# Performance work log

Measured on AMD Instinct MI355X. Metric: run time of the kernel, lower is better.

Reference implementation:

```python
import jax, jax.numpy as jnp
import numpy as np

N = 50000      # num nodes
E = 600000     # num edges (avg degree 12)
IN = 256       # in_feats
H = 128        # h_feats
P = 2          # prop_step
LN_EPS = 1e-5


def setup_inputs() -> dict:
    key = jax.random.key(0)
    ks = jax.random.split(key, 8)
    return {
        "in_feat": jax.random.normal(ks[0], (N, IN), jnp.float32),
        "row": jax.random.randint(ks[1], (E,), 0, N),  # target node of each edge
        "col": jax.random.randint(ks[2], (E,), 0, N),  # source node of each edge
        "lin_w": jax.random.normal(ks[3], (H, IN), jnp.float32) / np.sqrt(IN).astype(np.float32),
        "lin_b": jnp.zeros((H,), jnp.float32),
        "conv_w": jax.random.normal(ks[4], (H, H), jnp.float32) / np.sqrt(H).astype(np.float32),
        "conv_b": jnp.zeros((H,), jnp.float32),
        "root_emb": jax.random.normal(ks[5], (1, H), jnp.float32) * 0.02,
        "ln_gamma": jnp.ones((P, H), jnp.float32),
        "ln_beta": jnp.zeros((P, H), jnp.float32),
    }


def _layernorm(x, g, b):
    mu = jnp.mean(x, axis=-1, keepdims=True)
    var = jnp.mean(jnp.square(x - mu), axis=-1, keepdims=True)
    return (x - mu) * jax.lax.rsqrt(var + LN_EPS) * g + b


def reference(in_feat, row, col, lin_w, lin_b, conv_w, conv_b, root_emb, ln_gamma, ln_beta):
    n = in_feat.shape[0]
    h = in_feat @ lin_w.T + lin_b                      # [N, H]

    # OGB-style degree norm with +1 trick (original edges, row = target)
    deg = jax.ops.segment_sum(jnp.ones_like(row, dtype=h.dtype), row, num_segments=n) + 1.0
    deg_inv = 1.0 / deg                                # deg >= 1, never inf

    # GCNConv symmetric norm with self loops: D^-1/2 (A+I) D^-1/2
    loop = jnp.arange(n)
    r2 = jnp.concatenate([row, loop])                  # [E+N] targets
    c2 = jnp.concatenate([col, loop])                  # [E+N] sources
    d2 = jax.ops.segment_sum(jnp.ones_like(r2, dtype=h.dtype), r2, num_segments=n)
    dis = jnp.where(d2 > 0, jax.lax.rsqrt(jnp.maximum(d2, 1.0)), 0.0)
    ew = dis[r2] * dis[c2]                             # [E+N] edge weights

    root = root_emb[0]                                 # [H]
    ori = h
    for i in range(P):
        if i != 0:
            h = h + ori                                # residual
            h = _layernorm(h, ln_gamma[i], ln_beta[i])
            h = jax.nn.relu(h)
            # dropout=0.0 -> identity
        xw = h @ conv_w.T                              # [N, H]
        h_msg = jax.ops.segment_sum(ew[:, None] * xw[c2], r2, num_segments=n) + conv_b
        root_contrib = jax.nn.relu(h + root) * deg_inv[:, None]
        h = h_msg + root_contrib
    return h
```

## Files before the change

kernel.cpp:

```cpp
#include <hip/hip_runtime.h>

#define NN 50000
#define EE 600000
#define INF 256
#define HF 128

typedef __attribute__((ext_vector_type(8))) short short8;
typedef __attribute__((ext_vector_type(4))) float floatx4;

__device__ __forceinline__ unsigned short f32_to_bf16_rne(float x) {
    unsigned int u = __float_as_uint(x);
    unsigned int r = (u + 0x7FFFu + ((u >> 16) & 1u)) >> 16;
    return (unsigned short)r;
}
__device__ __forceinline__ float bf16_to_f32(unsigned short h) {
    return __uint_as_float(((unsigned int)h) << 16);
}
__device__ __forceinline__ float bf16lo_u32(unsigned int u) {
    return __uint_as_float(u << 16);
}
__device__ __forceinline__ float bf16hi_u32(unsigned int u) {
    return __uint_as_float(u & 0xFFFF0000u);
}

__global__ void count_deg(const int* __restrict__ row, int* __restrict__ cnt, int E) {
    int e = blockIdx.x * blockDim.x + threadIdx.x;
    if (e < E) atomicAdd(&cnt[row[e]], 1);
}

__global__ void scan_phase1(const int* __restrict__ cnt, int* __restrict__ bsum, int n) {
    __shared__ int sdata[256];
    int t = threadIdx.x;
    int i = blockIdx.x * 256 + t;
    sdata[t] = (i < n) ? cnt[i] : 0;
    __syncthreads();
    for (int s = 128; s > 0; s >>= 1) {
        if (t < s) sdata[t] += sdata[t + s];
        __syncthreads();
    }
    if (t == 0) bsum[blockIdx.x] = sdata[0];
}

__global__ void scan_phase2(int* __restrict__ bsum, int nb) {
    __shared__ int sdata[256];
    int t = threadIdx.x;
    int v = (t < nb) ? bsum[t] : 0;
    sdata[t] = v;
    __syncthreads();
    for (int s = 1; s < 256; s <<= 1) {
        int add = (t >= s) ? sdata[t - s] : 0;
        __syncthreads();
        sdata[t] += add;
        __syncthreads();
    }
    if (t < nb) bsum[t] = sdata[t] - v;
}

__global__ void scan_phase3(const int* __restrict__ cnt, const int* __restrict__ bsum,
                            int* __restrict__ row_start, int* __restrict__ fill_pos,
                            float* __restrict__ deg_inv, float* __restrict__ dis,
                            int n, int E) {
    __shared__ int sdata[256];
    int t = threadIdx.x;
    int i = blockIdx.x * 256 + t;
    int v = (i < n) ? cnt[i] : 0;
    sdata[t] = v;
    __syncthreads();
    for (int s = 1; s < 256; s <<= 1) {
        int add = (t >= s) ? sdata[t - s] : 0;
        __syncthreads();
        sdata[t] += add;
        __syncthreads();
    }
    if (i < n) {
        int ex = bsum[blockIdx.x] + sdata[t] - v;
        row_start[i] = ex;
        fill_pos[i] = ex;
        float d = (float)(v + 1);
        deg_inv[i] = 1.0f / d;
        dis[i] = rsqrtf(d);
    }
    if (blockIdx.x == 0 && t == 0) row_start[n] = E;
}

__global__ void fill_csr(const int* __restrict__ row, const int* __restrict__ col,
                         const float* __restrict__ dis, int* __restrict__ fill_pos,
                         int* __restrict__ csr_col, float* __restrict__ csr_wc, int E) {
    int e = blockIdx.x * blockDim.x + threadIdx.x;
    if (e < E) {
        int r = row[e];
        int c = col[e];
        int p = atomicAdd(&fill_pos[r], 1);
        csr_col[p] = c;
        csr_wc[p] = dis[c];
    }
}

__global__ void prepack_w(const float* __restrict__ lw, const float* __restrict__ cw,
                          unsigned short* __restrict__ wlh, unsigned short* __restrict__ wll,
                          unsigned short* __restrict__ wch, unsigned short* __restrict__ wcl) {
    int idx = blockIdx.x * blockDim.x + threadIdx.x;
    const float* src;
    unsigned short *dh, *dl;
    int i;
    if (idx < 8192) {
        src = lw; dh = wlh; dl = wll; i = idx;
    } else if (idx < 12288) {
        src = cw; dh = wch; dl = wcl; i = idx - 8192;
    } else return;
    float4 v = *reinterpret_cast<const float4*>(&src[i * 4]);
    unsigned short hx = f32_to_bf16_rne(v.x), hy = f32_to_bf16_rne(v.y),
                   hz = f32_to_bf16_rne(v.z), hw = f32_to_bf16_rne(v.w);
    ushort4 hp = {hx, hy, hz, hw};
    ushort4 lp = {f32_to_bf16_rne(v.x - bf16_to_f32(hx)), f32_to_bf16_rne(v.y - bf16_to_f32(hy)),
                  f32_to_bf16_rne(v.z - bf16_to_f32(hz)), f32_to_bf16_rne(v.w - bf16_to_f32(hw))};
    *reinterpret_cast<ushort4*>(&dh[i * 4]) = hp;
    *reinterpret_cast<ushort4*>(&dl[i * 4]) = lp;
}

template <int K, int MODE>
__global__ __launch_bounds__(256) void gemm_mfma(
    const float* __restrict__ Af,
    const unsigned short* __restrict__ Ahg, const unsigned short* __restrict__ Alg,
    const unsigned short* __restrict__ Whg, const unsigned short* __restrict__ Wlg,
    const float* __restrict__ bias,
    float* __restrict__ C, unsigned short* __restrict__ Cbf,
    const float* __restrict__ h, const float* __restrict__ deg_inv,
    const float* __restrict__ root,
    const float* __restrict__ gamma, const float* __restrict__ beta,
    int M) {
    constexpr int LDA = 40;
    __shared__ unsigned short Ah[64 * LDA];
    __shared__ unsigned short Al[64 * LDA];
    __shared__ unsigned short Wh[128 * LDA];
    __shared__ unsigned short Wl[128 * LDA];

    const int t = threadIdx.x;
    const int bm = blockIdx.x * 64;
    const int wave = t >> 6;
    const int lane = t & 63;
    const int lrow = lane & 15;
    const int quad = lane >> 4;
    const int kbase = quad * 8;

    floatx4 acc[8];
#pragma unroll
    for (int nt = 0; nt < 8; ++nt) acc[nt] = (floatx4){0.f, 0.f, 0.f, 0.f};

    for (int k0 = 0; k0 < K; k0 += 32) {
        if (MODE == 0) {
#pragma unroll
            for (int r = 0; r < 2; ++r) {
                int f = t + 256 * r;
                int rw = f >> 3;
                int cq = f & 7;
                float4 v = make_float4(0.f, 0.f, 0.f, 0.f);
                int gr = bm + rw;
                if (gr < M) v = *reinterpret_cast<const float4*>(&Af[(size_t)gr * K + k0 + cq * 4]);
                unsigned short hx = f32_to_bf16_rne(v.x), hy = f32_to_bf16_rne(v.y),
                               hz = f32_to_bf16_rne(v.z), hw = f32_to_bf16_rne(v.w);
                unsigned short lx = f32_to_bf16_rne(v.x - bf16_to_f32(hx)),
                               ly = f32_to_bf16_rne(v.y - bf16_to_f32(hy)),
                               lz = f32_to_bf16_rne(v.z - bf16_to_f32(hz)),
                               lw = f32_to_bf16_rne(v.w - bf16_to_f32(hw));
                uint2 hp, lp;
                hp.x = (unsigned)hx | ((unsigned)hy << 16);
                hp.y = (unsigned)hz | ((unsigned)hw << 16);
                lp.x = (unsigned)lx | ((unsigned)ly << 16);
                lp.y = (unsigned)lz | ((unsigned)lw << 16);
                *reinterpret_cast<uint2*>(&Ah[rw * LDA + cq * 4]) = hp;
                *reinterpret_cast<uint2*>(&Al[rw * LDA + cq * 4]) = lp;
            }
        } else {
            int rw = t >> 2;
            int cq = t & 3;
            int gr = bm + rw;
            uint4 hv = make_uint4(0, 0, 0, 0), lv = make_uint4(0, 0, 0, 0);
            if (gr < M) {
                hv = *reinterpret_cast<const uint4*>(&Ahg[(size_t)gr * K + k0 + cq * 8]);
                lv = *reinterpret_cast<const uint4*>(&Alg[(size_t)gr * K + k0 + cq * 8]);
            }
            *reinterpret_cast<uint2*>(&Ah[rw * LDA + cq * 8]) = make_uint2(hv.x, hv.y);
            *reinterpret_cast<uint2*>(&Ah[rw * LDA + cq * 8 + 4]) = make_uint2(hv.z, hv.w);
            *reinterpret_cast<uint2*>(&Al[rw * LDA + cq * 8]) = make_uint2(lv.x, lv.y);
            *reinterpret_cast<uint2*>(&Al[rw * LDA + cq * 8 + 4]) = make_uint2(lv.z, lv.w);
        }
#pragma unroll
        for (int r = 0; r < 2; ++r) {
            int f = t + 256 * r;
            int rw = f >> 2;
            int cq = f & 3;
            uint4 hv = *reinterpret_cast<const uint4*>(&Whg[(size_t)rw * K + k0 + cq * 8]);
            uint4 lv = *reinterpret_cast<const uint4*>(&Wlg[(size_t)rw * K + k0 + cq * 8]);
            *reinterpret_cast<uint2*>(&Wh[rw * LDA + cq * 8]) = make_uint2(hv.x, hv.y);
            *reinterpret_cast<uint2*>(&Wh[rw * LDA + cq * 8 + 4]) = make_uint2(hv.z, hv.w);
            *reinterpret_cast<uint2*>(&Wl[rw * LDA + cq * 8]) = make_uint2(lv.x, lv.y);
            *reinterpret_cast<uint2*>(&Wl[rw * LDA + cq * 8 + 4]) = make_uint2(lv.z, lv.w);
        }
        __syncthreads();

        short8 afh = *reinterpret_cast<const short8*>(&Ah[(wave * 16 + lrow) * LDA + kbase]);
        short8 afl = *reinterpret_cast<const short8*>(&Al[(wave * 16 + lrow) * LDA + kbase]);
        short8 bfh[8], bfl[8];
#pragma unroll
        for (int nt = 0; nt < 8; ++nt) {
            int rw = nt * 16 + lrow;
            bfh[nt] = *reinterpret_cast<const short8*>(&Wh[rw * LDA + kbase]);
            bfl[nt] = *reinterpret_cast<const short8*>(&Wl[rw * LDA + kbase]);
        }
#pragma unroll
        for (int nt = 0; nt < 8; ++nt) {
            acc[nt] = __builtin_amdgcn_mfma_f32_16x16x32_bf16(afh, bfh[nt], acc[nt], 0, 0, 0);
            acc[nt] = __builtin_amdgcn_mfma_f32_16x16x32_bf16(afl, bfh[nt], acc[nt], 0, 0, 0);
            acc[nt] = __builtin_amdgcn_mfma_f32_16x16x32_bf16(afh, bfl[nt], acc[nt], 0, 0, 0);
        }
        __syncthreads();
    }

    float cb[8], rt[8], gm[8], bt[8];
#pragma unroll
    for (int nt = 0; nt < 8; ++nt) {
        int colh = nt * 16 + lrow;
        cb[nt] = bias[colh];
        if (MODE >= 1) rt[nt] = root[colh];
        if (MODE == 1) { gm[nt] = gamma[colh]; bt[nt] = beta[colh]; }
    }

#pragma unroll
    for (int r = 0; r < 4; ++r) {
        int grow = bm + wave * 16 + quad * 4 + r;
        if (grow >= M) continue;
        float x[8];
        if (MODE == 0) {
#pragma unroll
            for (int nt = 0; nt < 8; ++nt) x[nt] = acc[nt][r] + cb[nt];
        } else {
            float di = deg_inv[grow];
            float hv[8];
#pragma unroll
            for (int nt = 0; nt < 8; ++nt) hv[nt] = h[(size_t)grow * HF + nt * 16 + lrow];
#pragma unroll
            for (int nt = 0; nt < 8; ++nt) {
                float v = acc[nt][r] + cb[nt] + fmaxf(hv[nt] + rt[nt], 0.f) * di;
                x[nt] = (MODE == 1) ? v + hv[nt] : v;
            }
        }
        if (MODE == 1) {
            float s = 0.f;
#pragma unroll
            for (int nt = 0; nt < 8; ++nt) s += x[nt];
#pragma unroll
            for (int m = 1; m < 16; m <<= 1) s += __shfl_xor(s, m, 64);
            float mu = s * (1.0f / HF);
            float var = 0.f;
#pragma unroll
            for (int nt = 0; nt < 8; ++nt) { float d = x[nt] - mu; var += d * d; }
#pragma unroll
            for (int m = 1; m < 16; m <<= 1) var += __shfl_xor(var, m, 64);
            float rs = rsqrtf(var * (1.0f / HF) + 1e-5f);
#pragma unroll
            for (int nt = 0; nt < 8; ++nt) {
                int colh = nt * 16 + lrow;
                float y = fmaxf((x[nt] - mu) * rs * gm[nt] + bt[nt], 0.f);
                C[(size_t)grow * HF + colh] = y;
                Cbf[(size_t)grow * HF + colh] = f32_to_bf16_rne(y);
            }
        } else if (MODE == 0) {
#pragma unroll
            for (int nt = 0; nt < 8; ++nt) {
                int colh = nt * 16 + lrow;
                C[(size_t)grow * HF + colh] = x[nt];
                Cbf[(size_t)grow * HF + colh] = f32_to_bf16_rne(x[nt]);
            }
        } else {
#pragma unroll
            for (int nt = 0; nt < 8; ++nt)
                C[(size_t)grow * HF + nt * 16 + lrow] = x[nt];
        }
    }
}

__global__ void aggregate(const int* __restrict__ row_start, const int* __restrict__ csr_col,
                          const float* __restrict__ csr_wc, const float* __restrict__ dis,
                          const float* __restrict__ deg_inv, const float* __restrict__ h,
                          const unsigned short* __restrict__ hbf,
                          unsigned short* __restrict__ agg_hi, unsigned short* __restrict__ agg_lo,
                          int n) {
    int wid = (blockIdx.x * blockDim.x + threadIdx.x) >> 6;
    int lane = threadIdx.x & 63;
    if (wid >= n) return;
    int q = lane >> 4;
    int l16 = lane & 15;
    int s = row_start[wid];
    int e = row_start[wid + 1];
    float a0 = 0.f, a1 = 0.f, a2 = 0.f, a3 = 0.f, a4 = 0.f, a5 = 0.f, a6 = 0.f, a7 = 0.f;
    for (int j = s + q; j < e; j += 4) {
        int c = csr_col[j];
        float wc = csr_wc[j];
        uint4 hv = *reinterpret_cast<const uint4*>(&hbf[(size_t)c * HF + l16 * 8]);
        a0 = fmaf(wc, bf16lo_u32(hv.x), a0);
        a1 = fmaf(wc, bf16hi_u32(hv.x), a1);
        a2 = fmaf(wc, bf16lo_u32(hv.y), a2);
        a3 = fmaf(wc, bf16hi_u32(hv.y), a3);
        a4 = fmaf(wc, bf16lo_u32(hv.z), a4);
        a5 = fmaf(wc, bf16hi_u32(hv.z), a5);
        a6 = fmaf(wc, bf16lo_u32(hv.w), a6);
        a7 = fmaf(wc, bf16hi_u32(hv.w), a7);
    }
#pragma unroll
    for (int m = 16; m < 64; m <<= 1) {
        a0 += __shfl_xor(a0, m, 64);
        a1 += __shfl_xor(a1, m, 64);
        a2 += __shfl_xor(a2, m, 64);
        a3 += __shfl_xor(a3, m, 64);
        a4 += __shfl_xor(a4, m, 64);
        a5 += __shfl_xor(a5, m, 64);
        a6 += __shfl_xor(a6, m, 64);
        a7 += __shfl_xor(a7, m, 64);
    }
    if (q == 0) {
        float dn = dis[wid];
        float di = deg_inv[wid];
        float4 hA = *reinterpret_cast<const float4*>(&h[(size_t)wid * HF + l16 * 8]);
        float4 hB = *reinterpret_cast<const float4*>(&h[(size_t)wid * HF + l16 * 8 + 4]);
        float o[8];
        o[0] = fmaf(dn, a0, di * hA.x);
        o[1] = fmaf(dn, a1, di * hA.y);
        o[2] = fmaf(dn, a2, di * hA.z);
        o[3] = fmaf(dn, a3, di * hA.w);
        o[4] = fmaf(dn, a4, di * hB.x);
        o[5] = fmaf(dn, a5, di * hB.y);
        o[6] = fmaf(dn, a6, di * hB.z);
        o[7] = fmaf(dn, a7, di * hB.w);
        unsigned short hi[8], lo[8];
#pragma unroll
        for (int k = 0; k < 8; ++k) {
            hi[k] = f32_to_bf16_rne(o[k]);
            lo[k] = f32_to_bf16_rne(o[k] - bf16_to_f32(hi[k]));
        }
        uint4 hp, lp;
        hp.x = (unsigned)hi[0] | ((unsigned)hi[1] << 16);
        hp.y = (unsigned)hi[2] | ((unsigned)hi[3] << 16);
        hp.z = (unsigned)hi[4] | ((unsigned)hi[5] << 16);
        hp.w = (unsigned)hi[6] | ((unsigned)hi[7] << 16);
        lp.x = (unsigned)lo[0] | ((unsigned)lo[1] << 16);
        lp.y = (unsigned)lo[2] | ((unsigned)lo[3] << 16);
        lp.z = (unsigned)lo[4] | ((unsigned)lo[5] << 16);
        lp.w = (unsigned)lo[6] | ((unsigned)lo[7] << 16);
        *reinterpret_cast<uint4*>(&agg_hi[(size_t)wid * HF + l16 * 8]) = hp;
        *reinterpret_cast<uint4*>(&agg_lo[(size_t)wid * HF + l16 * 8]) = lp;
    }
}

extern "C" void kernel_launch(void* const* d_in, const int* in_sizes, int n_in,
                              void* d_out, int out_size, void* d_ws, size_t ws_size,
                              hipStream_t stream) {
    const int N = NN, E = EE;
    const float* in_feat = (const float*)d_in[0];
    const int* row = (const int*)d_in[1];
    const int* col = (const int*)d_in[2];
    const float* lin_w = (const float*)d_in[3];
    const float* lin_b = (const float*)d_in[4];
    const float* conv_w = (const float*)d_in[5];
    const float* conv_b = (const float*)d_in[6];
    const float* root_emb = (const float*)d_in[7];
    const float* ln_gamma = (const float*)d_in[8];
    const float* ln_beta = (const float*)d_in[9];
    float* out = (float*)d_out;

    float* ws = (float*)d_ws;
    float* deg_inv = ws;
    float* dis = deg_inv + N;
    int* cnt = (int*)(dis + N);
    int* row_start = cnt + N;
    int* fill_pos = row_start + N + 4;
    int* bsum = fill_pos + N;
    int* csr_col = bsum + 256;
    float* csr_wc = (float*)(csr_col + E);
    unsigned short* wlh = (unsigned short*)(csr_wc + E);
    unsigned short* wll = wlh + 32768;
    unsigned short* wch = wll + 32768;
    unsigned short* wcl = wch + 16384;
    float* h0 = (float*)(wcl + 16384);
    unsigned short* hbf = (unsigned short*)(h0 + (size_t)N * HF);
    unsigned short* agg_hi = hbf + (size_t)N * HF;
    unsigned short* agg_lo = agg_hi + (size_t)N * HF;

    const int NB = (N + 255) / 256;

    hipMemsetAsync(cnt, 0, N * sizeof(int), stream);
    count_deg<<<(E + 255) / 256, 256, 0, stream>>>(row, cnt, E);
    scan_phase1<<<NB, 256, 0, stream>>>(cnt, bsum, N);
    scan_phase2<<<1, 256, 0, stream>>>(bsum, NB);
    scan_phase3<<<NB, 256, 0, stream>>>(cnt, bsum, row_start, fill_pos, deg_inv, dis, N, E);
    fill_csr<<<(E + 255) / 256, 256, 0, stream>>>(row, col, dis, fill_pos, csr_col, csr_wc, E);
    prepack_w<<<48, 256, 0, stream>>>(lin_w, conv_w, wlh, wll, wch, wcl);

    const int GB = (N + 63) / 64;
    const int WB = (N + 3) / 4;

    gemm_mfma<INF, 0><<<GB, 256, 0, stream>>>(in_feat, nullptr, nullptr, wlh, wll, lin_b,
                                              h0, hbf, nullptr, nullptr, nullptr,
                                              nullptr, nullptr, N);

    aggregate<<<WB, 256, 0, stream>>>(row_start, csr_col, csr_wc, dis, deg_inv, h0, hbf,
                                      agg_hi, agg_lo, N);
    gemm_mfma<HF, 1><<<GB, 256, 0, stream>>>(nullptr, agg_hi, agg_lo, wch, wcl, conv_b,
                                             h0, hbf, h0, deg_inv, root_emb,
                                             ln_gamma + HF, ln_beta + HF, N);

    aggregate<<<WB, 256, 0, stream>>>(row_start, csr_col, csr_wc, dis, deg_inv, h0, hbf,
                                      agg_hi, agg_lo, N);
    gemm_mfma<HF, 2><<<GB, 256, 0, stream>>>(nullptr, agg_hi, agg_lo, wch, wcl, conv_b,
                                             out, nullptr, h0, deg_inv, root_emb,
                                             nullptr, nullptr, N);
}
```

Baseline: 326.3 us.

## Prepack weights in MFMA fragment order, drop LDS staging, fold source norm into bf16

The weights are prepacked into MFMA B-fragment order so each lane loads its fragment directly from global memory. The GEMM stops staging through LDS and drops its block barriers, and each wave reads its A rows straight from global. The dis[c] source-side normalization moves into the bf16 copy written by the GEMM epilogue, so aggregation does plain sums and the per-edge csr_wc array is removed. In exchange, weight fragments are re-read from global/L2 by every wave, and the source scaling now happens before bf16 rounding.

```diff
diff --git a/kernel.cpp b/kernel.cpp
--- a/kernel.cpp
+++ b/kernel.cpp
@@ -21,6 +21,18 @@
 }
 __device__ __forceinline__ float bf16hi_u32(unsigned int u) {
     return __uint_as_float(u & 0xFFFF0000u);
+}
+__device__ __forceinline__ void cvt_hilo8(float4 v0, float4 v1, short8& hs, short8& ls) {
+    float x[8] = {v0.x, v0.y, v0.z, v0.w, v1.x, v1.y, v1.z, v1.w};
+    union { short8 s; unsigned short u[8]; } H, L;
+#pragma unroll
+    for (int k = 0; k < 8; ++k) {
+        unsigned short hi = f32_to_bf16_rne(x[k]);
+        H.u[k] = hi;
+        L.u[k] = f32_to_bf16_rne(x[k] - bf16_to_f32(hi));
+    }
+    hs = H.s;
+    ls = L.s;
 }
 
 __global__ void count_deg(const int* __restrict__ row, int* __restrict__ cnt, int E) {
@@ -84,137 +96,88 @@
 }
 
 __global__ void fill_csr(const int* __restrict__ row, const int* __restrict__ col,
-                         const float* __restrict__ dis, int* __restrict__ fill_pos,
-                         int* __restrict__ csr_col, float* __restrict__ csr_wc, int E) {
+                         int* __restrict__ fill_pos, int* __restrict__ csr_col, int E) {
     int e = blockIdx.x * blockDim.x + threadIdx.x;
     if (e < E) {
         int r = row[e];
-        int c = col[e];
         int p = atomicAdd(&fill_pos[r], 1);
-        csr_col[p] = c;
-        csr_wc[p] = dis[c];
+        csr_col[p] = col[e];
     }
 }
 
 __global__ void prepack_w(const float* __restrict__ lw, const float* __restrict__ cw,
-                          unsigned short* __restrict__ wlh, unsigned short* __restrict__ wll,
-                          unsigned short* __restrict__ wch, unsigned short* __restrict__ wcl) {
+                          unsigned short* __restrict__ flh, unsigned short* __restrict__ fll,
+                          unsigned short* __restrict__ fch, unsigned short* __restrict__ fcl) {
     int idx = blockIdx.x * blockDim.x + threadIdx.x;
     const float* src;
     unsigned short *dh, *dl;
-    int i;
-    if (idx < 8192) {
-        src = lw; dh = wlh; dl = wll; i = idx;
-    } else if (idx < 12288) {
-        src = cw; dh = wch; dl = wcl; i = idx - 8192;
+    int K, i;
+    if (idx < 4096) {
+        src = lw; dh = flh; dl = fll; K = INF; i = idx;
+    } else if (idx < 6144) {
+        src = cw; dh = fch; dl = fcl; K = HF; i = idx - 4096;
     } else return;
-    float4 v = *reinterpret_cast<const float4*>(&src[i * 4]);
-    unsigned short hx = f32_to_bf16_rne(v.x), hy = f32_to_bf16_rne(v.y),
-                   hz = f32_to_bf16_rne(v.z), hw = f32_to_bf16_rne(v.w);
-    ushort4 hp = {hx, hy, hz, hw};
-    ushort4 lp = {f32_to_bf16_rne(v.x - bf16_to_f32(hx)), f32_to_bf16_rne(v.y - bf16_to_f32(hy)),
-                  f32_to_bf16_rne(v.z - bf16_to_f32(hz)), f32_to_bf16_rne(v.w - bf16_to_f32(hw))};
-    *reinterpret_cast<ushort4*>(&dh[i * 4]) = hp;
-    *reinterpret_cast<ushort4*>(&dl[i * 4]) = lp;
+    int lane = i & 63;
+    int nt = (i >> 6) & 7;
+    int kc = i >> 9;
+    int rw = nt * 16 + (lane & 15);
+    int koff = kc * 32 + (lane >> 4) * 8;
+    const float* p = &src[(size_t)rw * K + koff];
+    float4 v0 = *reinterpret_cast<const float4*>(p);
+    float4 v1 = *reinterpret_cast<const float4*>(p + 4);
+    short8 hs, ls;
+    cvt_hilo8(v0, v1, hs, ls);
+    *reinterpret_cast<short8*>(&dh[(size_t)i * 8]) = hs;
+    *reinterpret_cast<short8*>(&dl[(size_t)i * 8]) = ls;
 }
 
 template <int K, int MODE>
-__global__ __launch_bounds__(256) void gemm_mfma(
+__global__ __launch_bounds__(256) void gemm_nolds(
     const float* __restrict__ Af,
     const unsigned short* __restrict__ Ahg, const unsigned short* __restrict__ Alg,
-    const unsigned short* __restrict__ Whg, const unsigned short* __restrict__ Wlg,
+    const unsigned short* __restrict__ Wfh, const unsigned short* __restrict__ Wfl,
     const float* __restrict__ bias,
     float* __restrict__ C, unsigned short* __restrict__ Cbf,
     const float* __restrict__ h, const float* __restrict__ deg_inv,
-    const float* __restrict__ root,
+    const float* __restrict__ dis, const float* __restrict__ root,
     const float* __restrict__ gamma, const float* __restrict__ beta,
     int M) {
-    constexpr int LDA = 40;
-    __shared__ unsigned short Ah[64 * LDA];
-    __shared__ unsigned short Al[64 * LDA];
-    __shared__ unsigned short Wh[128 * LDA];
-    __shared__ unsigned short Wl[128 * LDA];
-
     const int t = threadIdx.x;
-    const int bm = blockIdx.x * 64;
     const int wave = t >> 6;
     const int lane = t & 63;
     const int lrow = lane & 15;
     const int quad = lane >> 4;
-    const int kbase = quad * 8;
+    const int bm = blockIdx.x * 64;
+    int arow = bm + wave * 16 + lrow;
+    if (arow >= M) arow = M - 1;
 
     floatx4 acc[8];
 #pragma unroll
     for (int nt = 0; nt < 8; ++nt) acc[nt] = (floatx4){0.f, 0.f, 0.f, 0.f};
 
-    for (int k0 = 0; k0 < K; k0 += 32) {
+#pragma unroll 2
+    for (int kc = 0; kc < K / 32; ++kc) {
+        short8 afh, afl;
         if (MODE == 0) {
-#pragma unroll
-            for (int r = 0; r < 2; ++r) {
-                int f = t + 256 * r;
-                int rw = f >> 3;
-                int cq = f & 7;
-                float4 v = make_float4(0.f, 0.f, 0.f, 0.f);
-                int gr = bm + rw;
-                if (gr < M) v = *reinterpret_cast<const float4*>(&Af[(size_t)gr * K + k0 + cq * 4]);
-                unsigned short hx = f32_to_bf16_rne(v.x), hy = f32_to_bf16_rne(v.y),
-                               hz = f32_to_bf16_rne(v.z), hw = f32_to_bf16_rne(v.w);
-                unsigned short lx = f32_to_bf16_rne(v.x - bf16_to_f32(hx)),
-                               ly = f32_to_bf16_rne(v.y - bf16_to_f32(hy)),
-                               lz = f32_to_bf16_rne(v.z - bf16_to_f32(hz)),
-                               lw = f32_to_bf16_rne(v.w - bf16_to_f32(hw));
-                uint2 hp, lp;
-                hp.x = (unsigned)hx | ((unsigned)hy << 16);
-                hp.y = (unsigned)hz | ((unsigned)hw << 16);
-                lp.x = (unsigned)lx | ((unsigned)ly << 16);
-                lp.y = (unsigned)lz | ((unsigned)lw << 16);
-                *reinterpret_cast<uint2*>(&Ah[rw * LDA + cq * 4]) = hp;
-                *reinterpret_cast<uint2*>(&Al[rw * LDA + cq * 4]) = lp;
-            }
+            const float* ap = &Af[(size_t)arow * K + kc * 32 + quad * 8];
+            float4 a0 = *reinterpret_cast<const float4*>(ap);
+            float4 a1 = *reinterpret_cast<const float4*>(ap + 4);
+            cvt_hilo8(a0, a1, afh, afl);
         } else {
-            int rw = t >> 2;
-            int cq = t & 3;
-            int gr = bm + rw;
-            uint4 hv = make_uint4(0, 0, 0, 0), lv = make_uint4(0, 0, 0, 0);
-            if (gr < M) {
-                hv = *reinterpret_cast<const uint4*>(&Ahg[(size_t)gr * K + k0 + cq * 8]);
-                lv = *reinterpret_cast<const uint4*>(&Alg[(size_t)gr * K + k0 + cq * 8]);
-            }
-            *reinterpret_cast<uint2*>(&Ah[rw * LDA + cq * 8]) = make_uint2(hv.x, hv.y);
-            *reinterpret_cast<uint2*>(&Ah[rw * LDA + cq * 8 + 4]) = make_uint2(hv.z, hv.w);
-            *reinterpret_cast<uint2*>(&Al[rw * LDA + cq * 8]) = make_uint2(lv.x, lv.y);
-            *reinterpret_cast<uint2*>(&Al[rw * LDA + cq * 8 + 4]) = make_uint2(lv.z, lv.w);
-        }
-#pragma unroll
-        for (int r = 0; r < 2; ++r) {
-            int f = t + 256 * r;
-            int rw = f >> 2;
-            int cq = f & 3;
-            uint4 hv = *reinterpret_cast<const uint4*>(&Whg[(size_t)rw * K + k0 + cq * 8]);
-            uint4 lv = *reinterpret_cast<const uint4*>(&Wlg[(size_t)rw * K + k0 + cq * 8]);
-            *reinterpret_cast<uint2*>(&Wh[rw * LDA + cq * 8]) = make_uint2(hv.x, hv.y);
-            *reinterpret_cast<uint2*>(&Wh[rw * LDA + cq * 8 + 4]) = make_uint2(hv.z, hv.w);
-            *reinterpret_cast<uint2*>(&Wl[rw * LDA + cq * 8]) = make_uint2(lv.x, lv.y);
-            *reinterpret_cast<uint2*>(&Wl[rw * LDA + cq * 8 + 4]) = make_uint2(lv.z, lv.w);
-        }
-        __syncthreads();
-
-        short8 afh = *reinterpret_cast<const short8*>(&Ah[(wave * 16 + lrow) * LDA + kbase]);
-        short8 afl = *reinterpret_cast<const short8*>(&Al[(wave * 16 + lrow) * LDA + kbase]);
-        short8 bfh[8], bfl[8];
+            size_t ao = (size_t)arow * K + kc * 32 + quad * 8;
+            afh = *reinterpret_cast<const short8*>(&Ahg[ao]);
+            afl = *reinterpret_cast<const short8*>(&Alg[ao]);
+        }
+        const unsigned short* wh = &Wfh[(size_t)kc * 4096 + lane * 8];
+        const unsigned short* wl = &Wfl[(size_t)kc * 4096 + lane * 8];
 #pragma unroll
         for (int nt = 0; nt < 8; ++nt) {
-            int rw = nt * 16 + lrow;
-            bfh[nt] = *reinterpret_cast<const short8*>(&Wh[rw * LDA + kbase]);
-            bfl[nt] = *reinterpret_cast<const short8*>(&Wl[rw * LDA + kbase]);
-        }
-#pragma unroll
-        for (int nt = 0; nt < 8; ++nt) {
-            acc[nt] = __builtin_amdgcn_mfma_f32_16x16x32_bf16(afh, bfh[nt], acc[nt], 0, 0, 0);
-            acc[nt] = __builtin_amdgcn_mfma_f32_16x16x32_bf16(afl, bfh[nt], acc[nt], 0, 0, 0);
-            acc[nt] = __builtin_amdgcn_mfma_f32_16x16x32_bf16(afh, bfl[nt], acc[nt], 0, 0, 0);
-        }
-        __syncthreads();
+            short8 bfh = *reinterpret_cast<const short8*>(wh + nt * 512);
+            short8 bfl = *reinterpret_cast<const short8*>(wl + nt * 512);
+            acc[nt] = __builtin_amdgcn_mfma_f32_16x16x32_bf16(afh, bfh, acc[nt], 0, 0, 0);
+            acc[nt] = __builtin_amdgcn_mfma_f32_16x16x32_bf16(afl, bfh, acc[nt], 0, 0, 0);
+            acc[nt] = __builtin_amdgcn_mfma_f32_16x16x32_bf16(afh, bfl, acc[nt], 0, 0, 0);
+        }
     }
 
     float cb[8], rt[8], gm[8], bt[8];
@@ -229,16 +192,17 @@
 #pragma unroll
     for (int r = 0; r < 4; ++r) {
         int grow = bm + wave * 16 + quad * 4 + r;
-        if (grow >= M) continue;
+        bool ok = (grow < M);
+        int gr = ok ? grow : M - 1;
         float x[8];
         if (MODE == 0) {
 #pragma unroll
             for (int nt = 0; nt < 8; ++nt) x[nt] = acc[nt][r] + cb[nt];
         } else {
-            float di = deg_inv[grow];
+            float di = deg_inv[gr];
             float hv[8];
 #pragma unroll
-            for (int nt = 0; nt < 8; ++nt) hv[nt] = h[(size_t)grow * HF + nt * 16 + lrow];
+            for (int nt = 0; nt < 8; ++nt) hv[nt] = h[(size_t)gr * HF + nt * 16 + lrow];
 #pragma unroll
             for (int nt = 0; nt < 8; ++nt) {
                 float v = acc[nt][r] + cb[nt] + fmaxf(hv[nt] + rt[nt], 0.f) * di;
@@ -258,32 +222,39 @@
 #pragma unroll
             for (int m = 1; m < 16; m <<= 1) var += __shfl_xor(var, m, 64);
             float rs = rsqrtf(var * (1.0f / HF) + 1e-5f);
-#pragma unroll
-            for (int nt = 0; nt < 8; ++nt) {
-                int colh = nt * 16 + lrow;
-                float y = fmaxf((x[nt] - mu) * rs * gm[nt] + bt[nt], 0.f);
-                C[(size_t)grow * HF + colh] = y;
-                Cbf[(size_t)grow * HF + colh] = f32_to_bf16_rne(y);
+            float ds = dis[gr];
+            if (ok) {
+#pragma unroll
+                for (int nt = 0; nt < 8; ++nt) {
+                    int colh = nt * 16 + lrow;
+                    float y = fmaxf((x[nt] - mu) * rs * gm[nt] + bt[nt], 0.f);
+                    C[(size_t)grow * HF + colh] = y;
+                    Cbf[(size_t)grow * HF + colh] = f32_to_bf16_rne(ds * y);
+                }
             }
         } else if (MODE == 0) {
-#pragma unroll
-            for (int nt = 0; nt < 8; ++nt) {
-                int colh = nt * 16 + lrow;
-                C[(size_t)grow * HF + colh] = x[nt];
-                Cbf[(size_t)grow * HF + colh] = f32_to_bf16_rne(x[nt]);
+            if (ok) {
+                float ds = dis[grow];
+#pragma unroll
+                for (int nt = 0; nt < 8; ++nt) {
+                    int colh = nt * 16 + lrow;
+                    C[(size_t)grow * HF + colh] = x[nt];
+                    Cbf[(size_t)grow * HF + colh] = f32_to_bf16_rne(ds * x[nt]);
+                }
             }
         } else {
-#pragma unroll
-            for (int nt = 0; nt < 8; ++nt)
-                C[(size_t)grow * HF + nt * 16 + lrow] = x[nt];
+            if (ok) {
+#pragma unroll
+                for (int nt = 0; nt < 8; ++nt)
+                    C[(size_t)grow * HF + nt * 16 + lrow] = x[nt];
+            }
         }
     }
 }
 
 __global__ void aggregate(const int* __restrict__ row_start, const int* __restrict__ csr_col,
-                          const float* __restrict__ csr_wc, const float* __restrict__ dis,
-                          const float* __restrict__ deg_inv, const float* __restrict__ h,
-                          const unsigned short* __restrict__ hbf,
+                          const float* __restrict__ dis, const float* __restrict__ deg_inv,
+                          const float* __restrict__ h, const unsigned short* __restrict__ hbf,
                           unsigned short* __restrict__ agg_hi, unsigned short* __restrict__ agg_lo,
                           int n) {
     int wid = (blockIdx.x * blockDim.x + threadIdx.x) >> 6;
@@ -296,16 +267,15 @@
     float a0 = 0.f, a1 = 0.f, a2 = 0.f, a3 = 0.f, a4 = 0.f, a5 = 0.f, a6 = 0.f, a7 = 0.f;
     for (int j = s + q; j < e; j += 4) {
         int c = csr_col[j];
-        float wc = csr_wc[j];
         uint4 hv = *reinterpret_cast<const uint4*>(&hbf[(size_t)c * HF + l16 * 8]);
-        a0 = fmaf(wc, bf16lo_u32(hv.x), a0);
-        a1 = fmaf(wc, bf16hi_u32(hv.x), a1);
-        a2 = fmaf(wc, bf16lo_u32(hv.y), a2);
-        a3 = fmaf(wc, bf16hi_u32(hv.y), a3);
-        a4 = fmaf(wc, bf16lo_u32(hv.z), a4);
-        a5 = fmaf(wc, bf16hi_u32(hv.z), a5);
-        a6 = fmaf(wc, bf16lo_u32(hv.w), a6);
-        a7 = fmaf(wc, bf16hi_u32(hv.w), a7);
+        a0 += bf16lo_u32(hv.x);
+        a1 += bf16hi_u32(hv.x);
+        a2 += bf16lo_u32(hv.y);
+        a3 += bf16hi_u32(hv.y);
+        a4 += bf16lo_u32(hv.z);
+        a5 += bf16hi_u32(hv.z);
+        a6 += bf16lo_u32(hv.w);
+        a7 += bf16hi_u32(hv.w);
     }
 #pragma unroll
     for (int m = 16; m < 64; m <<= 1) {
@@ -369,22 +339,23 @@
     float* out = (float*)d_out;
 
     float* ws = (float*)d_ws;
-    float* deg_inv = ws;
-    float* dis = deg_inv + N;
-    int* cnt = (int*)(dis + N);
-    int* row_start = cnt + N;
-    int* fill_pos = row_start + N + 4;
-    int* bsum = fill_pos + N;
-    int* csr_col = bsum + 256;
-    float* csr_wc = (float*)(csr_col + E);
-    unsigned short* wlh = (unsigned short*)(csr_wc + E);
-    unsigned short* wll = wlh + 32768;
-    unsigned short* wch = wll + 32768;
-    unsigned short* wcl = wch + 16384;
-    float* h0 = (float*)(wcl + 16384);
-    unsigned short* hbf = (unsigned short*)(h0 + (size_t)N * HF);
-    unsigned short* agg_hi = hbf + (size_t)N * HF;
-    unsigned short* agg_lo = agg_hi + (size_t)N * HF;
+    size_t o = 0;
+    float* deg_inv = ws + o; o += N;
+    float* dis = ws + o; o += N;
+    int* cnt = (int*)(ws + o); o += N;
+    int* row_start = (int*)(ws + o); o += N + 4;
+    int* fill_pos = (int*)(ws + o); o += N;
+    int* bsum = (int*)(ws + o); o += 256;
+    int* csr_col = (int*)(ws + o); o += E;
+    o = (o + 3) & ~(size_t)3;
+    unsigned short* flh = (unsigned short*)(ws + o); o += 16384;
+    unsigned short* fll = (unsigned short*)(ws + o); o += 16384;
+    unsigned short* fch = (unsigned short*)(ws + o); o += 8192;
+    unsigned short* fcl = (unsigned short*)(ws + o); o += 8192;
+    float* h0 = ws + o; o += (size_t)N * HF;
+    unsigned short* hbf = (unsigned short*)(ws + o); o += (size_t)N * HF / 2;
+    unsigned short* agg_hi = (unsigned short*)(ws + o); o += (size_t)N * HF / 2;
+    unsigned short* agg_lo = (unsigned short*)(ws + o); o += (size_t)N * HF / 2;
 
     const int NB = (N + 255) / 256;
 
@@ -393,25 +364,25 @@
     scan_phase1<<<NB, 256, 0, stream>>>(cnt, bsum, N);
     scan_phase2<<<1, 256, 0, stream>>>(bsum, NB);
     scan_phase3<<<NB, 256, 0, stream>>>(cnt, bsum, row_start, fill_pos, deg_inv, dis, N, E);
-    fill_csr<<<(E + 255) / 256, 256, 0, stream>>>(row, col, dis, fill_pos, csr_col, csr_wc, E);
-    prepack_w<<<48, 256, 0, stream>>>(lin_w, conv_w, wlh, wll, wch, wcl);
+    fill_csr<<<(E + 255) / 256, 256, 0, stream>>>(row, col, fill_pos, csr_col, E);
+    prepack_w<<<24, 256, 0, stream>>>(lin_w, conv_w, flh, fll, fch, fcl);
 
     const int GB = (N + 63) / 64;
     const int WB = (N + 3) / 4;
 
-    gemm_mfma<INF, 0><<<GB, 256, 0, stream>>>(in_feat, nullptr, nullptr, wlh, wll, lin_b,
-                                              h0, hbf, nullptr, nullptr, nullptr,
+    gemm_nolds<INF, 0><<<GB, 256, 0, stream>>>(in_feat, nullptr, nullptr, flh, fll, lin_b,
+                                               h0, hbf, nullptr, nullptr, dis, nullptr,
+                                               nullptr, nullptr, N);
+
+    aggregate<<<WB, 256, 0, stream>>>(row_start, csr_col, dis, deg_inv, h0, hbf,
+                                      agg_hi, agg_lo, N);
+    gemm_nolds<HF, 1><<<GB, 256, 0, stream>>>(nullptr, agg_hi, agg_lo, fch, fcl, conv_b,
+                                              h0, hbf, h0, deg_inv, dis, root_emb,
+                                              ln_gamma + HF, ln_beta + HF, N);
+
+    aggregate<<<WB, 256, 0, stream>>>(row_start, csr_col, dis, deg_inv, h0, hbf,
+                                      agg_hi, agg_lo, N);
+    gemm_nolds<HF, 2><<<GB, 256, 0, stream>>>(nullptr, agg_hi, agg_lo, fch, fcl, conv_b,
+                                              out, nullptr, h0, deg_inv, dis, root_emb,
                                               nullptr, nullptr, N);
-
-    aggregate<<<WB, 256, 0, stream>>>(row_start, csr_col, csr_wc, dis, deg_inv, h0, hbf,
-                                      agg_hi, agg_lo, N);
-    gemm_mfma<HF, 1><<<GB, 256, 0, stream>>>(nullptr, agg_hi, agg_lo, wch, wcl, conv_b,
-                                             h0, hbf, h0, deg_inv, root_emb,
-                                             ln_gamma + HF, ln_beta + HF, N);
-
-    aggregate<<<WB, 256, 0, stream>>>(row_start, csr_col, csr_wc, dis, deg_inv, h0, hbf,
-                                      agg_hi, agg_lo, N);
-    gemm_mfma<HF, 2><<<GB, 256, 0, stream>>>(nullptr, agg_hi, agg_lo, wch, wcl, conv_b,
-                                             out, nullptr, h0, deg_inv, root_emb,
-                                             nullptr, nullptr, N);
-}
+}
```

Result: no change. 331.6 us (+1.6%).
